# Optimization experiments

Measured on AMD Instinct MI355X. Metric: run time of the kernel, lower is better.

Reference implementation:

```python
import jax, jax.numpy as jnp
import numpy as np

B, S, D_IN, D_OUT = 4, 2048, 1024, 1024

def setup_inputs() -> dict:
    key = jax.random.key(0)
    kx, kq, kk, kv = jax.random.split(key, 4)
    x = jax.random.normal(kx, (B, S, D_IN), dtype=jnp.float32)
    scale = 1.0 / np.sqrt(D_IN)
    Wq = jax.random.normal(kq, (D_IN, D_OUT), dtype=jnp.float32) * scale
    Wk = jax.random.normal(kk, (D_IN, D_OUT), dtype=jnp.float32) * scale
    Wv = jax.random.normal(kv, (D_IN, D_OUT), dtype=jnp.float32) * scale
    return {"x": x, "Wq": Wq, "Wk": Wk, "Wv": Wv}

def reference(x, Wq, Wk, Wv):
    # x: [B, S, d_in]; Linear without bias -> x @ W
    q = jnp.einsum('bsd,de->bse', x, Wq)
    k = jnp.einsum('bsd,de->bse', x, Wk)
    v = jnp.einsum('bsd,de->bse', x, Wv)
    S_len = x.shape[1]
    scores = jnp.einsum('bqe,bke->bqk', q, k)  # [B, S, S]
    causal = jnp.triu(jnp.ones((S_len, S_len), dtype=bool), k=1)
    scores = jnp.where(causal[None, :, :], -jnp.inf, scores)
    inv_sqrt_d = jnp.asarray(1.0 / np.sqrt(k.shape[-1]), dtype=scores.dtype)
    weights = jax.nn.softmax(scores * inv_sqrt_d, axis=-1)
    # dropout=0.0 -> identity
    return jnp.einsum('bqk,bke->bqe', weights, v)
```

## Files before the change

kernel.cpp:

```cpp
#include <hip/hip_runtime.h>
#include <cstdint>

#define DEV __device__ __forceinline__

typedef unsigned short u16;
typedef unsigned int   u32;
typedef __bf16 bf16x8 __attribute__((ext_vector_type(8)));
typedef float  f32x4  __attribute__((ext_vector_type(4)));

static constexpr int BATCH = 4;
static constexpr int SEQ   = 2048;
static constexpr int DMODEL= 1024;
static constexpr int MPROJ = BATCH * SEQ;

DEV u16 f2bf(float f) {
    u32 u = __float_as_uint(f);
    u32 r = (u + 0x7FFFu + ((u >> 16) & 1u)) >> 16;
    return (u16)r;
}
DEV float bf2f(u16 u) { return __uint_as_float(((u32)u) << 16); }

DEV void async16(const void* g, void* l) {
    __builtin_amdgcn_global_load_lds(
        (__attribute__((address_space(1))) void*)(g),
        (__attribute__((address_space(3))) void*)(l),
        16, 0, 0);
}

__global__ void conv_x_kernel(const float* __restrict__ x, u16* __restrict__ xb, int n8) {
    int i = blockIdx.x * blockDim.x + threadIdx.x;
    if (i >= n8) return;
    const float4* p = (const float4*)x + (size_t)i * 2;
    float4 a = p[0], b = p[1];
    uint4 o;
    o.x = (u32)f2bf(a.x) | ((u32)f2bf(a.y) << 16);
    o.y = (u32)f2bf(a.z) | ((u32)f2bf(a.w) << 16);
    o.z = (u32)f2bf(b.x) | ((u32)f2bf(b.y) << 16);
    o.w = (u32)f2bf(b.z) | ((u32)f2bf(b.w) << 16);
    ((uint4*)xb)[i] = o;
}

__global__ void convW_kernel(const float* __restrict__ Wq, const float* __restrict__ Wk,
                             const float* __restrict__ Wv, u16* __restrict__ Wt) {
    __shared__ u16 tile[32][33];
    int z = blockIdx.z;
    const float* src = (z == 0) ? Wq : (z == 1 ? Wk : Wv);
    u16* dst = Wt + (size_t)z * DMODEL * DMODEL;
    int k0 = blockIdx.x * 32, n0 = blockIdx.y * 32;
    int tx = threadIdx.x, ty = threadIdx.y;
    #pragma unroll
    for (int j = 0; j < 4; ++j)
        tile[ty + j * 8][tx] = f2bf(src[(size_t)(k0 + ty + j * 8) * DMODEL + n0 + tx]);
    __syncthreads();
    #pragma unroll
    for (int j = 0; j < 4; ++j)
        dst[(size_t)(n0 + ty + j * 8) * DMODEL + k0 + tx] = tile[tx][ty + j * 8];
}

__global__ void transV_kernel(const u16* __restrict__ V, u16* __restrict__ Vt) {
    __shared__ u16 tile[32][33];
    int b = blockIdx.z;
    int s0 = blockIdx.x * 32, d0 = blockIdx.y * 32;
    const u16* src = V + (size_t)b * SEQ * DMODEL;
    u16* dst = Vt + (size_t)b * DMODEL * SEQ;
    int tx = threadIdx.x, ty = threadIdx.y;
    #pragma unroll
    for (int j = 0; j < 4; ++j)
        tile[ty + j * 8][tx] = src[(size_t)(s0 + ty + j * 8) * DMODEL + d0 + tx];
    __syncthreads();
    #pragma unroll
    for (int j = 0; j < 4; ++j)
        dst[(size_t)(d0 + ty + j * 8) * SEQ + s0 + tx] = tile[tx][ty + j * 8];
}

__global__ __launch_bounds__(256)
void gemm_bt(const u16* __restrict__ A, const u16* __restrict__ Bt, u16* __restrict__ C,
             int N, int K, int NB, long sA, long sB, long sC) {
    __shared__ __bf16 lsA[128 * 32];
    __shared__ __bf16 lsB[128 * 32];

    int bx = blockIdx.x, b = blockIdx.y;
    { int q = (int)(gridDim.x >> 3); bx = (bx & 7) * q + (bx >> 3); }
    int mb = bx / NB, nb = bx % NB;
    const u16* Ab = A + (size_t)b * sA;
    const u16* Bb = Bt + (size_t)b * sB;
    u16* Cb = C + (size_t)b * sC;

    const int m0 = mb * 128, n0 = nb * 128;
    const int tid = threadIdx.x, wid = tid >> 6, lane = tid & 63;
    const int wm = (wid >> 1) * 64, wn = (wid & 1) * 64;

    const char* gA = (const char*)(Ab + (size_t)(m0 + wid * 32 + (lane >> 2)) * K) + (lane & 3) * 16;
    const char* gB = (const char*)(Bb + (size_t)(n0 + wid * 32 + (lane >> 2)) * K) + (lane & 3) * 16;
    const long rowskip = (long)16 * K * 2;
    __bf16* lA0 = &lsA[wid * 1024];
    __bf16* lB0 = &lsB[wid * 1024];

    f32x4 zero = {0.f, 0.f, 0.f, 0.f};
    f32x4 acc[4][4];
    #pragma unroll
    for (int i = 0; i < 4; ++i)
        #pragma unroll
        for (int j = 0; j < 4; ++j) acc[i][j] = zero;

    const int aoff = (wm + (lane & 15)) * 32 + (lane >> 4) * 8;
    const int boff = (wn + (lane & 15)) * 32 + (lane >> 4) * 8;

    const int nkt = K >> 5;
    for (int kt = 0; kt < nkt; ++kt) {
        __syncthreads();
        async16(gA, lA0);            async16(gA + rowskip, lA0 + 512);
        async16(gB, lB0);            async16(gB + rowskip, lB0 + 512);
        gA += 64; gB += 64;
        __syncthreads();

        bf16x8 af[4], bf[4];
        #pragma unroll
        for (int i = 0; i < 4; ++i)
            af[i] = *reinterpret_cast<const bf16x8*>(&lsA[aoff + i * 512]);
        #pragma unroll
        for (int i = 0; i < 4; ++i)
            bf[i] = *reinterpret_cast<const bf16x8*>(&lsB[boff + i * 512]);

        #pragma unroll
        for (int mi = 0; mi < 4; ++mi)
            #pragma unroll
            for (int ni = 0; ni < 4; ++ni)
                acc[mi][ni] = __builtin_amdgcn_mfma_f32_16x16x32_bf16(
                    af[mi], bf[ni], acc[mi][ni], 0, 0, 0);
    }

    const int crow0 = m0 + wm + ((lane >> 4) << 2);
    const int ccol0 = n0 + wn + (lane & 15);
    #pragma unroll
    for (int mi = 0; mi < 4; ++mi)
        #pragma unroll
        for (int ni = 0; ni < 4; ++ni)
            #pragma unroll
            for (int j = 0; j < 4; ++j)
                Cb[(size_t)(crow0 + mi * 16 + j) * N + (ccol0 + ni * 16)] =
                    f2bf(acc[mi][ni][j]);
}

template <int EPI, bool TRI, bool CK>
__global__ __launch_bounds__(256)
void gemm_db(const u16* __restrict__ A, const u16* __restrict__ Bt, void* __restrict__ Cv,
             int N, int K, int NB, long sA, long sB, long sC, float scale,
             float* __restrict__ lsum) {
    __shared__ __bf16 lsA[2][128 * 64];
    __shared__ __bf16 lsB[2][128 * 64];

    int bx = blockIdx.x, b = blockIdx.y;
    { int q = (int)(gridDim.x >> 3); bx = (bx & 7) * q + (bx >> 3); }
    int mb, nb;
    if (TRI) {
        int t = bx;
        int r = (int)((sqrtf(8.f * (float)t + 1.f) - 1.f) * 0.5f);
        while ((r + 1) * (r + 2) / 2 <= t) ++r;
        while (r * (r + 1) / 2 > t) --r;
        mb = r; nb = t - r * (r + 1) / 2;
    } else {
        mb = bx / NB; nb = bx % NB;
    }
    const u16* Ab = A + (size_t)b * sA;
    const u16* Bb = Bt + (size_t)b * sB;

    const int m0 = mb * 128, n0 = nb * 128;
    const int keff = CK ? min(K, (mb + 1) * 128) : K;

    const int tid = threadIdx.x, wid = tid >> 6, lane = tid & 63;
    const int wm = (wid >> 1) * 64, wn = (wid & 1) * 64;

    const int srow = wid * 32 + (lane >> 3);
    const int scol = (((lane & 7) ^ (lane >> 3)) << 4);
    const char* gA = (const char*)(Ab + (size_t)(m0 + srow) * K) + scol;
    const char* gB = (const char*)(Bb + (size_t)(n0 + srow) * K) + scol;
    const long rowskip8 = (long)8 * K * 2;

    f32x4 zero = {0.f, 0.f, 0.f, 0.f};
    f32x4 acc[4][4];
    #pragma unroll
    for (int i = 0; i < 4; ++i)
        #pragma unroll
        for (int j = 0; j < 4; ++j) acc[i][j] = zero;

    const int arow = wm + (lane & 15);
    const int brow = wn + (lane & 15);
    const int swz  = (lane & 7) << 4;
    const int cb0  = ((lane >> 4) << 4);

#define STAGE_DB(kt, dd)                                                      \
    {                                                                         \
        const char* pa_ = gA + (size_t)(kt) * 128;                            \
        const char* pb_ = gB + (size_t)(kt) * 128;                            \
        _Pragma("unroll")                                                     \
        for (int i_ = 0; i_ < 4; ++i_) {                                      \
            async16(pa_ + i_ * rowskip8, &lsA[dd][(wid * 32 + i_ * 8) * 64]); \
            async16(pb_ + i_ * rowskip8, &lsB[dd][(wid * 32 + i_ * 8) * 64]); \
        }                                                                     \
    }

    const int nkt = keff >> 6;
    STAGE_DB(0, 0);
    __syncthreads();

    int d = 0;
    for (int kt = 0; kt < nkt; ++kt) {
        if (kt + 1 < nkt) STAGE_DB(kt + 1, d ^ 1);

        const char* baseA = (const char*)lsA[d];
        const char* baseB = (const char*)lsB[d];
        bf16x8 af[2][4], bf[2][4];
        #pragma unroll
        for (int ks = 0; ks < 2; ++ks) {
            const int cbs = (ks * 64 + cb0) ^ swz;
            #pragma unroll
            for (int mi = 0; mi < 4; ++mi)
                af[ks][mi] = *(const bf16x8*)(baseA + (size_t)(arow + mi * 16) * 128 + cbs);
            #pragma unroll
            for (int ni = 0; ni < 4; ++ni)
                bf[ks][ni] = *(const bf16x8*)(baseB + (size_t)(brow + ni * 16) * 128 + cbs);
        }

        __builtin_amdgcn_s_setprio(1);
        #pragma unroll
        for (int mi = 0; mi < 4; ++mi)
            #pragma unroll
            for (int ni = 0; ni < 4; ++ni) {
                acc[mi][ni] = __builtin_amdgcn_mfma_f32_16x16x32_bf16(
                    af[0][mi], bf[0][ni], acc[mi][ni], 0, 0, 0);
                acc[mi][ni] = __builtin_amdgcn_mfma_f32_16x16x32_bf16(
                    af[1][mi], bf[1][ni], acc[mi][ni], 0, 0, 0);
            }
        __builtin_amdgcn_s_setprio(0);

        __syncthreads();
        d ^= 1;
    }
#undef STAGE_DB

    const int crow0 = m0 + wm + ((lane >> 4) << 2);
    const int ccol0 = n0 + wn + (lane & 15);

    if constexpr (EPI == 1) {
        u16* Cb = (u16*)Cv + (size_t)b * sC;
        float* lb = lsum + (size_t)b * SEQ;
        #pragma unroll
        for (int mi = 0; mi < 4; ++mi)
            #pragma unroll
            for (int j = 0; j < 4; ++j) {
                const int crow = crow0 + mi * 16 + j;
                float rsum = 0.f;
                #pragma unroll
                for (int ni = 0; ni < 4; ++ni) {
                    const int ccol = ccol0 + ni * 16;
                    float e = (ccol <= crow) ? __expf(acc[mi][ni][j] * scale) : 0.f;
                    rsum += e;
                    Cb[(size_t)crow * N + ccol] = f2bf(e);
                }
                rsum += __shfl_xor(rsum, 1);
                rsum += __shfl_xor(rsum, 2);
                rsum += __shfl_xor(rsum, 4);
                rsum += __shfl_xor(rsum, 8);
                if ((lane & 15) == 0) atomicAdd(&lb[crow], rsum);
            }
    } else {
        float* Cb = (float*)Cv + (size_t)b * sC;
        const float* lb = lsum + (size_t)b * SEQ;
        #pragma unroll
        for (int mi = 0; mi < 4; ++mi)
            #pragma unroll
            for (int j = 0; j < 4; ++j) {
                const int crow = crow0 + mi * 16 + j;
                const float inv = 1.f / lb[crow];
                #pragma unroll
                for (int ni = 0; ni < 4; ++ni)
                    Cb[(size_t)crow * N + (ccol0 + ni * 16)] = acc[mi][ni][j] * inv;
            }
    }
}

extern "C" void kernel_launch(void* const* d_in, const int* in_sizes, int n_in,
                              void* d_out, int out_size, void* d_ws, size_t ws_size,
                              hipStream_t stream) {
    const float* x  = (const float*)d_in[0];
    const float* Wq = (const float*)d_in[1];
    const float* Wk = (const float*)d_in[2];
    const float* Wv = (const float*)d_in[3];
    float* out = (float*)d_out;

    char* w = (char*)d_ws;
    u16* xb = (u16*)(w);
    u16* Wt = (u16*)(w + (16L << 20));
    u16* Q  = (u16*)(w + (22L << 20));
    u16* Kb = (u16*)(w + (38L << 20));
    u16* V  = (u16*)(w + (54L << 20));
    u16* Vt = (u16*)(w + (70L << 20));
    u16* SP = (u16*)(w + (86L << 20));
    float* lsum = (float*)(w + (118L << 20));

    hipMemsetAsync(lsum, 0, (size_t)BATCH * SEQ * sizeof(float), stream);
    conv_x_kernel<<<(MPROJ * DMODEL / 8 + 255) / 256, 256, 0, stream>>>(x, xb, MPROJ * DMODEL / 8);
    convW_kernel<<<dim3(32, 32, 3), dim3(32, 8), 0, stream>>>(Wq, Wk, Wv, Wt);
    gemm_bt<<<dim3(512, 3), 256, 0, stream>>>(
        xb, Wt, Q, DMODEL, DMODEL, 8,
        0, (long)DMODEL * DMODEL, (long)MPROJ * DMODEL);
    transV_kernel<<<dim3(64, 32, 4), dim3(32, 8), 0, stream>>>(V, Vt);
    gemm_db<1, true, false><<<dim3(136, 4), 256, 0, stream>>>(
        Q, Kb, SP, SEQ, DMODEL, 0,
        (long)SEQ * DMODEL, (long)SEQ * DMODEL, (long)SEQ * SEQ, 0.03125f, lsum);
    gemm_db<2, false, true><<<dim3(128, 4), 256, 0, stream>>>(
        SP, Vt, out, DMODEL, SEQ, 8,
        (long)SEQ * SEQ, (long)DMODEL * SEQ, (long)SEQ * DMODEL, 1.f, lsum);
}
```

Measured before the change: 252.9 us.

## Replace QKV projection GEMM with 256x256 double-buffered 8-wave pipelined kernel

Replaces the simple 128x128 single-buffered projection GEMM with a 256x256-tile, 512-thread kernel. It uses double-buffered LDS, XOR-swizzled layout and a four-phase ping-pong schedule that overlaps async global-to-LDS prefetch with MFMA work. The aim is to raise arithmetic intensity, hide global load latency and cut LDS bank conflicts. The cost is 128KB of LDS per block and fewer blocks (384), which risks occupancy and wave-quantization losses.

```diff
diff --git a/kernel.cpp b/kernel.cpp
--- a/kernel.cpp
+++ b/kernel.cpp
@@ -73,73 +73,131 @@
         dst[(size_t)(d0 + ty + j * 8) * SEQ + s0 + tx] = tile[tx][ty + j * 8];
 }
 
-__global__ __launch_bounds__(256)
-void gemm_bt(const u16* __restrict__ A, const u16* __restrict__ Bt, u16* __restrict__ C,
-             int N, int K, int NB, long sA, long sB, long sC) {
-    __shared__ __bf16 lsA[128 * 32];
-    __shared__ __bf16 lsB[128 * 32];
+__global__ __launch_bounds__(512, 2)
+void gemm_8p(const u16* __restrict__ A, const u16* __restrict__ Bt, u16* __restrict__ C,
+             int N, int K, int NB, long sB, long sC) {
+    __shared__ __bf16 lsA[2][256 * 64];
+    __shared__ __bf16 lsB[2][256 * 64];
 
     int bx = blockIdx.x, b = blockIdx.y;
     { int q = (int)(gridDim.x >> 3); bx = (bx & 7) * q + (bx >> 3); }
-    int mb = bx / NB, nb = bx % NB;
-    const u16* Ab = A + (size_t)b * sA;
+    const int mb = bx / NB, nb = bx % NB;
+    const u16* Ab = A;
     const u16* Bb = Bt + (size_t)b * sB;
     u16* Cb = C + (size_t)b * sC;
-
-    const int m0 = mb * 128, n0 = nb * 128;
+    const int m0 = mb * 256, n0 = nb * 256;
+
     const int tid = threadIdx.x, wid = tid >> 6, lane = tid & 63;
-    const int wm = (wid >> 1) * 64, wn = (wid & 1) * 64;
-
-    const char* gA = (const char*)(Ab + (size_t)(m0 + wid * 32 + (lane >> 2)) * K) + (lane & 3) * 16;
-    const char* gB = (const char*)(Bb + (size_t)(n0 + wid * 32 + (lane >> 2)) * K) + (lane & 3) * 16;
-    const long rowskip = (long)16 * K * 2;
-    __bf16* lA0 = &lsA[wid * 1024];
-    __bf16* lB0 = &lsB[wid * 1024];
-
-    f32x4 zero = {0.f, 0.f, 0.f, 0.f};
-    f32x4 acc[4][4];
-    #pragma unroll
-    for (int i = 0; i < 4; ++i)
-        #pragma unroll
-        for (int j = 0; j < 4; ++j) acc[i][j] = zero;
-
-    const int aoff = (wm + (lane & 15)) * 32 + (lane >> 4) * 8;
-    const int boff = (wn + (lane & 15)) * 32 + (lane >> 4) * 8;
-
-    const int nkt = K >> 5;
+    const int wm = wid >> 2, wn = wid & 3;
+
+    const int srow  = tid >> 3;
+    const int scolb = ((tid & 7) ^ (srow & 7)) << 4;
+    const char* gA = (const char*)Ab + (size_t)(m0 + srow) * K * 2 + scolb;
+    const char* gB = (const char*)Bb + (size_t)(n0 + srow) * K * 2 + scolb;
+    const long risk = (long)64 * K * 2;
+
+#define STAGE_A(kt, dd) { _Pragma("unroll")                                   \
+    for (int i_ = 0; i_ < 4; ++i_)                                            \
+        async16(gA + (size_t)(kt) * 128 + i_ * risk,                          \
+                &lsA[dd][i_ * 4096 + wid * 512]); }
+#define STAGE_B(kt, dd) { _Pragma("unroll")                                   \
+    for (int i_ = 0; i_ < 4; ++i_)                                            \
+        async16(gB + (size_t)(kt) * 128 + i_ * risk,                          \
+                &lsB[dd][i_ * 4096 + wid * 512]); }
+
+    f32x4 acc[8][4];
+    #pragma unroll
+    for (int i = 0; i < 8; ++i)
+        #pragma unroll
+        for (int j = 0; j < 4; ++j) acc[i][j] = (f32x4){0.f, 0.f, 0.f, 0.f};
+
+    const int fr  = lane & 15;
+    const int cb0 = (lane >> 4) << 4;
+    const int swz = (lane & 7) << 4;
+
+    const int nkt = K >> 6;
+    STAGE_A(0, 0); STAGE_B(0, 0);
+    __syncthreads();
+
     for (int kt = 0; kt < nkt; ++kt) {
-        __syncthreads();
-        async16(gA, lA0);            async16(gA + rowskip, lA0 + 512);
-        async16(gB, lB0);            async16(gB + rowskip, lB0 + 512);
-        gA += 64; gB += 64;
-        __syncthreads();
-
-        bf16x8 af[4], bf[4];
-        #pragma unroll
-        for (int i = 0; i < 4; ++i)
-            af[i] = *reinterpret_cast<const bf16x8*>(&lsA[aoff + i * 512]);
-        #pragma unroll
-        for (int i = 0; i < 4; ++i)
-            bf[i] = *reinterpret_cast<const bf16x8*>(&lsB[boff + i * 512]);
-
+        const int d = kt & 1;
+        const bool pre = (kt + 1 < nkt);
+        const char* baseA = (const char*)lsA[d];
+        const char* baseB = (const char*)lsB[d];
+        bf16x8 afr[4][2], bfr[4][2];
+
+        #pragma unroll
+        for (int p = 0; p < 4; ++p) {
+            const int ms = p >> 1, ns = p & 1;
+            if (p == 0) {
+                #pragma unroll
+                for (int mi = 0; mi < 4; ++mi) {
+                    const size_t r = (size_t)(wm * 128 + mi * 16 + fr) * 128;
+                    #pragma unroll
+                    for (int ks = 0; ks < 2; ++ks)
+                        afr[mi][ks] = *(const bf16x8*)(baseA + r + ((ks * 64 + cb0) ^ swz));
+                }
+                #pragma unroll
+                for (int nn = 0; nn < 4; ++nn) {
+                    const size_t r = (size_t)(wn * 64 + nn * 16 + fr) * 128;
+                    #pragma unroll
+                    for (int ks = 0; ks < 2; ++ks)
+                        bfr[nn][ks] = *(const bf16x8*)(baseB + r + ((ks * 64 + cb0) ^ swz));
+                }
+            }
+            if (p == 2) {
+                #pragma unroll
+                for (int mi = 0; mi < 4; ++mi) {
+                    const size_t r = (size_t)(wm * 128 + 64 + mi * 16 + fr) * 128;
+                    #pragma unroll
+                    for (int ks = 0; ks < 2; ++ks)
+                        afr[mi][ks] = *(const bf16x8*)(baseA + r + ((ks * 64 + cb0) ^ swz));
+                }
+            }
+            if (p == 0 && pre) STAGE_A(kt + 1, d ^ 1);
+            if (p == 1 && pre) STAGE_B(kt + 1, d ^ 1);
+            if (p == 3) asm volatile("s_waitcnt vmcnt(0)" ::: "memory");
+            __builtin_amdgcn_sched_barrier(0);
+            __builtin_amdgcn_s_barrier();
+            asm volatile("s_waitcnt lgkmcnt(0)" ::: "memory");
+            __builtin_amdgcn_sched_barrier(0);
+            __builtin_amdgcn_s_setprio(1);
+            #pragma unroll
+            for (int mi = 0; mi < 4; ++mi)
+                #pragma unroll
+                for (int ni = 0; ni < 2; ++ni) {
+                    f32x4 a0 = acc[ms * 4 + mi][ns * 2 + ni];
+                    a0 = __builtin_amdgcn_mfma_f32_16x16x32_bf16(
+                        afr[mi][0], bfr[ns * 2 + ni][0], a0, 0, 0, 0);
+                    a0 = __builtin_amdgcn_mfma_f32_16x16x32_bf16(
+                        afr[mi][1], bfr[ns * 2 + ni][1], a0, 0, 0, 0);
+                    acc[ms * 4 + mi][ns * 2 + ni] = a0;
+                }
+            __builtin_amdgcn_s_setprio(0);
+            __builtin_amdgcn_sched_barrier(0);
+            __builtin_amdgcn_s_barrier();
+        }
+    }
+#undef STAGE_A
+#undef STAGE_B
+
+    const int crow0 = m0 + wm * 128 + ((lane >> 4) << 2);
+    const int ccol0 = n0 + wn * 64 + (lane & 15);
+    #pragma unroll
+    for (int ms = 0; ms < 2; ++ms)
         #pragma unroll
         for (int mi = 0; mi < 4; ++mi)
             #pragma unroll
-            for (int ni = 0; ni < 4; ++ni)
-                acc[mi][ni] = __builtin_amdgcn_mfma_f32_16x16x32_bf16(
-                    af[mi], bf[ni], acc[mi][ni], 0, 0, 0);
-    }
-
-    const int crow0 = m0 + wm + ((lane >> 4) << 2);
-    const int ccol0 = n0 + wn + (lane & 15);
-    #pragma unroll
-    for (int mi = 0; mi < 4; ++mi)
-        #pragma unroll
-        for (int ni = 0; ni < 4; ++ni)
-            #pragma unroll
-            for (int j = 0; j < 4; ++j)
-                Cb[(size_t)(crow0 + mi * 16 + j) * N + (ccol0 + ni * 16)] =
-                    f2bf(acc[mi][ni][j]);
+            for (int ns = 0; ns < 2; ++ns)
+                #pragma unroll
+                for (int ni = 0; ni < 2; ++ni)
+                    #pragma unroll
+                    for (int j = 0; j < 4; ++j) {
+                        const int crow = crow0 + ms * 64 + mi * 16 + j;
+                        const int ccol = ccol0 + ns * 32 + ni * 16;
+                        Cb[(size_t)crow * N + ccol] =
+                            f2bf(acc[ms * 4 + mi][ns * 2 + ni][j]);
+                    }
 }
 
 template <int EPI, bool TRI, bool CK>
@@ -302,9 +360,9 @@
     hipMemsetAsync(lsum, 0, (size_t)BATCH * SEQ * sizeof(float), stream);
     conv_x_kernel<<<(MPROJ * DMODEL / 8 + 255) / 256, 256, 0, stream>>>(x, xb, MPROJ * DMODEL / 8);
     convW_kernel<<<dim3(32, 32, 3), dim3(32, 8), 0, stream>>>(Wq, Wk, Wv, Wt);
-    gemm_bt<<<dim3(512, 3), 256, 0, stream>>>(
-        xb, Wt, Q, DMODEL, DMODEL, 8,
-        0, (long)DMODEL * DMODEL, (long)MPROJ * DMODEL);
+    gemm_8p<<<dim3(128, 3), 512, 0, stream>>>(
+        xb, Wt, Q, DMODEL, DMODEL, 4,
+        (long)DMODEL * DMODEL, (long)MPROJ * DMODEL);
     transV_kernel<<<dim3(64, 32, 4), dim3(32, 8), 0, stream>>>(V, Vt);
     gemm_db<1, true, false><<<dim3(136, 4), 256, 0, stream>>>(
         Q, Kb, SP, SEQ, DMODEL, 0,
```

After: 247.0 us. 1.02x faster.
